# Performance work log

Hardware: AMD Instinct MI355X
Metric: run time of the kernel (lower is better)

Reference implementation:

```python
import jax, jax.numpy as jnp
import numpy as np

WS = 2   # window_size
NH = 8   # num_heads


def window_attn(x, Wqkv, bqkv, scale, ws=WS, nh=NH):
    # x: (B, H, W, C) -> tiny ws*ws-token windowed MHA, faithful to torch reshape order
    B, H, W, C = x.shape
    hg, wg = H // ws, W // ws
    hd = C // nh
    xw = x.reshape(B, hg, ws, wg, ws, C).transpose(0, 1, 3, 2, 4, 5)  # (B,hg,wg,ws,ws,C)
    qkv = (xw @ Wqkv + bqkv).reshape(B, hg * wg, ws * ws, 3, nh, hd)
    q, k, v = jnp.transpose(qkv, (3, 0, 1, 4, 2, 5))  # each (B,G,nh,n,hd), n=ws*ws
    attn = jax.nn.softmax(jnp.einsum('bgnqd,bgnkd->bgnqk', q, k) * scale, axis=-1)
    o = jnp.einsum('bgnqk,bgnkd->bgnqd', attn, v)
    o = o.transpose(0, 1, 3, 2, 4).reshape(B, hg, wg, ws, ws, C)
    return o.transpose(0, 1, 3, 2, 4, 5).reshape(B, H, W, C)


def reference(x, Wqkv, bqkv, Wproj, bproj):
    B, C, H, W = x.shape
    scale = (C // NH) ** (-0.5)
    xr = x.reshape(B, H, W, C)  # raw reshape (NOT a transpose) -- faithful to source

    # --- Global path ---
    g = window_attn(xr, Wqkv, bqkv, scale) @ Wproj + bproj

    # --- Local path ---
    l = xr.reshape(B, C, H, W)                         # raw reshape, as in source
    l = l.reshape(B, C, H // 2, 2, W // 2, 2).mean(axis=(3, 5))  # AvgPool2d(2)
    h, w = H // 2, W // 2
    l = l.reshape(B, h, w, C)                          # raw reshape, as in source
    l = window_attn(l, Wqkv, bqkv, scale)
    l = l.reshape(B, C, h, w)                          # raw reshape, as in source
    # attn_x: reflect-pad top by 1, AvgPool2d((2,1), stride=1)
    px = jnp.pad(l, ((0, 0), (0, 0), (1, 0), (0, 0)), mode='reflect')
    lx = 0.5 * (px[:, :, :-1, :] + px[:, :, 1:, :])
    # attn_y: reflect-pad right by 1, AvgPool2d((1,2), stride=1)
    py = jnp.pad(l, ((0, 0), (0, 0), (0, 0), (0, 1)), mode='reflect')
    ly = 0.5 * (py[..., :-1] + py[..., 1:])
    # bilinear upsample x2, align_corners=False (half-pixel, matches jax.image.resize)
    l = jax.image.resize(lx + ly, (B, C, H, W), method='bilinear')
    l = l.reshape(B, H, W, C)                          # raw reshape, as in source

    return (g + l).transpose(0, 3, 1, 2)  # (B, C, H, W)


def setup_inputs() -> dict:
    key = jax.random.key(0)
    k1, k2, k3, k4, k5 = jax.random.split(key, 5)
    B, C, H, W = 4, 512, 128, 128
    x = jax.random.normal(k1, (B, C, H, W), dtype=jnp.float32)
    Wqkv = jax.random.normal(k2, (C, 3 * C), dtype=jnp.float32) * 0.02
    bqkv = jax.random.normal(k3, (3 * C,), dtype=jnp.float32) * 0.02
    Wproj = jax.random.normal(k4, (C, C), dtype=jnp.float32) * 0.02
    bproj = jax.random.normal(k5, (C,), dtype=jnp.float32) * 0.02
    return {'x': x, 'Wqkv': Wqkv, 'bqkv': bqkv, 'Wproj': Wproj, 'bproj': bproj}
```

## Files before the change

kernel.cpp:

```cpp
#include <hip/hip_runtime.h>

typedef float f32x4 __attribute__((ext_vector_type(4)));
typedef float f32x2 __attribute__((ext_vector_type(2)));
typedef __bf16 bf16x8 __attribute__((ext_vector_type(8)));
typedef __bf16 bf16x4 __attribute__((ext_vector_type(4)));

__device__ __forceinline__ void gll16(const void* g, void* l) {
  __builtin_amdgcn_global_load_lds(
      (const __attribute__((address_space(1))) uint32_t*)g,
      (__attribute__((address_space(3))) uint32_t*)l, 16, 0, 0);
}

__global__ __launch_bounds__(256) void gemm_bf16_k512(
    const __bf16* __restrict__ A, const __bf16* __restrict__ BT,
    const float* __restrict__ bias, __bf16* __restrict__ C, int N, int gx)
{
  __shared__ __bf16 sh[16384];
  __bf16* As = sh;
  __bf16* Bs = sh + 8192;
  const int tid = threadIdx.x;
  const int wave = tid >> 6, lane = tid & 63;
  const int wr = (wave >> 1) * 64, wc = (wave & 1) * 64;
  const int l15 = lane & 15, l4 = lane >> 4;

  int lin = blockIdx.x;
  int olin = (lin & 7) * ((int)gridDim.x >> 3) + (lin >> 3);
  int bn = olin % gx, bm = olin / gx;
  const long arow0 = (long)bm * 128;
  const long brow0 = (long)bn * 128;

  const int srow = wave * 8 + (lane >> 3);
  const int scp8 = (lane & 7) * 8;

  f32x4 acc[4][4] = {};

  for (int kt = 0; kt < 512; kt += 64) {
    #pragma unroll
    for (int i = 0; i < 4; i++) {
      int row = srow + i * 32;
      int gc = scp8 ^ ((row & 7) * 8);
      gll16(A  + (arow0 + row) * 512 + kt + gc, (char*)As + i * 4096 + wave * 1024);
      gll16(BT + (brow0 + row) * 512 + kt + gc, (char*)Bs + i * 4096 + wave * 1024);
    }
    __syncthreads();
    #pragma unroll
    for (int kk = 0; kk < 2; kk++) {
      bf16x8 af[4], bfr[4];
      #pragma unroll
      for (int m = 0; m < 4; m++) {
        int row = wr + m * 16 + l15;
        int cp8 = ((kk * 4 + l4) * 8) ^ ((row & 7) * 8);
        af[m] = *(const bf16x8*)&As[row * 64 + cp8];
      }
      #pragma unroll
      for (int n = 0; n < 4; n++) {
        int row = wc + n * 16 + l15;
        int cp8 = ((kk * 4 + l4) * 8) ^ ((row & 7) * 8);
        bfr[n] = *(const bf16x8*)&Bs[row * 64 + cp8];
      }
      #pragma unroll
      for (int m = 0; m < 4; m++)
        #pragma unroll
        for (int n = 0; n < 4; n++)
          acc[m][n] = __builtin_amdgcn_mfma_f32_16x16x32_bf16(bfr[n], af[m], acc[m][n], 0, 0, 0);
    }
    __syncthreads();
  }

  #pragma unroll
  for (int n = 0; n < 4; n++) {
    f32x4 bv = *(const f32x4*)(bias + brow0 + wc + n * 16 + l4 * 4);
    #pragma unroll
    for (int m = 0; m < 4; m++) {
      int row = wr + m * 16 + l15;
      int colb = (wc + n * 16 + l4 * 4) * 2;
      int byte = row * 256 + (colb ^ ((row & 7) << 4));
      bf16x4 o;
      #pragma unroll
      for (int k = 0; k < 4; k++) o[k] = (__bf16)(acc[m][n][k] + bv[k]);
      *(bf16x4*)((char*)sh + byte) = o;
    }
  }
  __syncthreads();
  {
    int row = tid >> 1;
    int halfs = (tid & 1) * 8;
    __bf16* gdst = C + (arow0 + row) * (long)N + brow0 + halfs * 8;
    #pragma unroll
    for (int k = 0; k < 8; k++) {
      int s = halfs + k;
      int slot = (s & 8) | ((s ^ row) & 7);
      bf16x8 v = *(const bf16x8*)((const char*)sh + row * 256 + slot * 16);
      *(bf16x8*)(gdst + k * 8) = v;
    }
  }
}

__global__ __launch_bounds__(256) void attn4(
    const __bf16* __restrict__ qkv, __bf16* __restrict__ o,
    int nwin, int wg, int Wimg, int wpb, int bst)
{
  int tid = blockIdx.x * 256 + threadIdx.x;
  int m = tid & 3;
  int head = (tid >> 2) & 7;
  int win = tid >> 5;
  if (win >= nwin) return;
  int b = win / wpb, wrm = win % wpb;
  int i = wrm / wg, j = wrm % wg;
  int t0 = b * bst + 2 * i * Wimg + 2 * j;
  int tn[4] = { t0, t0 + 1, t0 + Wimg, t0 + Wimg + 1 };
  int trow = tn[m];
  const int co = head * 64;

  float qf[64];
  #pragma unroll
  for (int c = 0; c < 8; c++) {
    bf16x8 v = *(const bf16x8*)(qkv + (long)trow * 1536 + co + c * 8);
    #pragma unroll
    for (int e = 0; e < 8; e++) qf[c * 8 + e] = (float)v[e];
  }

  float s[4];
  #pragma unroll
  for (int n = 0; n < 4; n++) {
    float acc = 0.f;
    #pragma unroll
    for (int c = 0; c < 8; c++) {
      bf16x8 kv = *(const bf16x8*)(qkv + (long)tn[n] * 1536 + 512 + co + c * 8);
      #pragma unroll
      for (int e = 0; e < 8; e++) acc += qf[c * 8 + e] * (float)kv[e];
    }
    s[n] = acc * 0.125f;
  }

  float mx = fmaxf(fmaxf(s[0], s[1]), fmaxf(s[2], s[3]));
  float e0 = __expf(s[0] - mx), e1 = __expf(s[1] - mx),
        e2 = __expf(s[2] - mx), e3 = __expf(s[3] - mx);
  float inv = 1.f / (e0 + e1 + e2 + e3);
  float w4[4] = { e0 * inv, e1 * inv, e2 * inv, e3 * inv };

  float of[64] = {};
  #pragma unroll
  for (int n = 0; n < 4; n++) {
    float wn = w4[n];
    #pragma unroll
    for (int c = 0; c < 8; c++) {
      bf16x8 vv = *(const bf16x8*)(qkv + (long)tn[n] * 1536 + 1024 + co + c * 8);
      #pragma unroll
      for (int e = 0; e < 8; e++) of[c * 8 + e] += wn * (float)vv[e];
    }
  }

  #pragma unroll
  for (int c = 0; c < 8; c++) {
    bf16x8 ov;
    #pragma unroll
    for (int e = 0; e < 8; e++) ov[e] = (__bf16)of[c * 8 + e];
    *(bf16x8*)(o + (long)trow * 512 + co + c * 8) = ov;
  }
}

__global__ __launch_bounds__(256) void transpose_f32_bf16(
    const float* __restrict__ in, __bf16* __restrict__ out, int K, int N)
{
  __shared__ float t[64][65];
  int n0 = blockIdx.x * 64, k0 = blockIdx.y * 64;
  int tid = threadIdx.x;
  int nl4 = (tid & 15) * 4, kl = tid >> 4;
  #pragma unroll
  for (int p = 0; p < 4; p++) {
    int kk = kl + p * 16;
    f32x4 v = *(const f32x4*)(in + (long)(k0 + kk) * N + n0 + nl4);
    t[kk][nl4 + 0] = v.x; t[kk][nl4 + 1] = v.y; t[kk][nl4 + 2] = v.z; t[kk][nl4 + 3] = v.w;
  }
  __syncthreads();
  int ks = tid & 63, wv = tid >> 6;
  #pragma unroll
  for (int p = 0; p < 16; p++) {
    int nn = wv * 16 + p;
    out[(long)(n0 + nn) * K + k0 + ks] = (__bf16)t[ks][nn];
  }
}

__global__ __launch_bounds__(256) void convpool(const float* __restrict__ x,
    __bf16* __restrict__ Xbf, __bf16* __restrict__ P)
{
  int t = blockIdx.x * 256 + threadIdx.x;
  int j8 = (t & 15) * 8;
  int i2 = (t >> 4) & 63;
  long bc = t >> 10;
  const float* r0 = x + bc * 16384 + (2 * i2) * 128 + j8;
  f32x4 a0 = *(const f32x4*)r0,         a1 = *(const f32x4*)(r0 + 4);
  f32x4 b0 = *(const f32x4*)(r0 + 128), b1 = *(const f32x4*)(r0 + 132);
  bf16x8 xa, xb;
  xa[0] = (__bf16)a0.x; xa[1] = (__bf16)a0.y; xa[2] = (__bf16)a0.z; xa[3] = (__bf16)a0.w;
  xa[4] = (__bf16)a1.x; xa[5] = (__bf16)a1.y; xa[6] = (__bf16)a1.z; xa[7] = (__bf16)a1.w;
  xb[0] = (__bf16)b0.x; xb[1] = (__bf16)b0.y; xb[2] = (__bf16)b0.z; xb[3] = (__bf16)b0.w;
  xb[4] = (__bf16)b1.x; xb[5] = (__bf16)b1.y; xb[6] = (__bf16)b1.z; xb[7] = (__bf16)b1.w;
  *(bf16x8*)(Xbf + bc * 16384 + (2 * i2) * 128 + j8) = xa;
  *(bf16x8*)(Xbf + bc * 16384 + (2 * i2) * 128 + 128 + j8) = xb;
  bf16x4 p;
  p[0] = (__bf16)((a0.x + a0.y + b0.x + b0.y) * 0.25f);
  p[1] = (__bf16)((a0.z + a0.w + b0.z + b0.w) * 0.25f);
  p[2] = (__bf16)((a1.x + a1.y + b1.x + b1.y) * 0.25f);
  p[3] = (__bf16)((a1.z + a1.w + b1.z + b1.w) * 0.25f);
  *(bf16x4*)(P + bc * 4096 + i2 * 64 + (t & 15) * 4) = p;
}

__global__ void skern(const __bf16* __restrict__ l, float* __restrict__ s)
{
  int tid = blockIdx.x * 256 + threadIdx.x;
  int j = tid & 63, i = (tid >> 6) & 63;
  long bc = tid >> 12;
  const __bf16* base = l + bc * 4096;
  int im1 = (i == 0) ? 1 : i - 1;
  int jp1 = (j == 63) ? 62 : j + 1;
  float v = 0.5f * (float)base[im1 * 64 + j] + (float)base[i * 64 + j]
          + 0.5f * (float)base[i * 64 + jp1];
  s[tid] = v;
}

__global__ __launch_bounds__(256) void final_v2(
    const __bf16* __restrict__ G, const float* __restrict__ S, float* __restrict__ out)
{
  __shared__ float Sl[8192];
  __shared__ float t[64][65];
  int b = blockIdx.z;
  int p0 = blockIdx.y * 64, c0 = blockIdx.x * 64;
  int tid = threadIdx.x;

  int k2 = blockIdx.y;
  const float* Sb = S + (long)b * 2097152 + (long)k2 * 8192;
  #pragma unroll
  for (int i = 0; i < 8; i++)
    *(f32x4*)&Sl[i * 1024 + tid * 4] = *(const f32x4*)(Sb + i * 1024 + tid * 4);
  __syncthreads();

  int cl4 = (tid & 15) * 4, pl = tid >> 4;
  const __bf16* Gb = G + ((long)b * 16384 + p0) * 512 + c0;
  #pragma unroll
  for (int q2 = 0; q2 < 4; q2++) {
    int pp = pl + q2 * 16;
    bf16x4 g = *(const bf16x4*)(Gb + (long)pp * 512 + cl4);
    int qbase = (p0 + pp) * 512 + c0 + cl4;
    #pragma unroll
    for (int e = 0; e < 4; e++) {
      int q = qbase + e;
      int lc = (q >> 14) & 1;
      int r = q & 16383, hh = r >> 7, ww = r & 127;
      const float* sb = Sl + lc * 4096;
      int i0, i1, j0, j1; float wi0, wi1, wj0, wj1;
      if (hh & 1) { i0 = hh >> 1; i1 = (i0 < 63) ? i0 + 1 : 63; wi0 = 0.75f; wi1 = 0.25f; }
      else        { i1 = hh >> 1; i0 = (i1 > 0) ? i1 - 1 : 0;   wi0 = 0.25f; wi1 = 0.75f; }
      if (ww & 1) { j0 = ww >> 1; j1 = (j0 < 63) ? j0 + 1 : 63; wj0 = 0.75f; wj1 = 0.25f; }
      else        { j1 = ww >> 1; j0 = (j1 > 0) ? j1 - 1 : 0;   wj0 = 0.25f; wj1 = 0.75f; }
      float up = wi0 * (wj0 * sb[i0 * 64 + j0] + wj1 * sb[i0 * 64 + j1])
               + wi1 * (wj0 * sb[i1 * 64 + j0] + wj1 * sb[i1 * 64 + j1]);
      t[pp][cl4 + e] = (float)g[e] + up;
    }
  }
  __syncthreads();
  int l15b = tid & 15, hi = (tid >> 4) & 3, wv = tid >> 6;
  float* ob = out + (long)b * 8388608 + (long)c0 * 16384 + p0;
  #pragma unroll
  for (int it = 0; it < 4; it++) {
    int cc = wv * 16 + it * 4 + hi;
    f32x4 v;
    v.x = t[l15b * 4 + 0][cc]; v.y = t[l15b * 4 + 1][cc];
    v.z = t[l15b * 4 + 2][cc]; v.w = t[l15b * 4 + 3][cc];
    *(f32x4*)(ob + (long)cc * 16384 + l15b * 4) = v;
  }
}

extern "C" void kernel_launch(void* const* d_in, const int* in_sizes, int n_in,
                              void* d_out, int out_size, void* d_ws, size_t ws_size,
                              hipStream_t stream)
{
  const float* x     = (const float*)d_in[0];
  const float* Wqkv  = (const float*)d_in[1];
  const float* bqkv  = (const float*)d_in[2];
  const float* Wproj = (const float*)d_in[3];
  const float* bproj = (const float*)d_in[4];
  float* out = (float*)d_out;

  char* w = (char*)d_ws;
  __bf16* WqkvT  = (__bf16*)w;  w += (size_t)1536 * 512 * 2;
  __bf16* WprojT = (__bf16*)w;  w += (size_t)512 * 512 * 2;
  __bf16* Xbf    = (__bf16*)w;  w += (size_t)65536 * 512 * 2;
  __bf16* G      = Xbf;
  __bf16* P      = (__bf16*)w;  w += (size_t)2048 * 4096 * 2;

  bool batched = ws_size >= ((size_t)356 << 20);
  size_t mchunk = batched ? 65536 : 16384;
  __bf16* QKVbuf = (__bf16*)w;  w += mchunk * 1536 * 2;
  __bf16* Obuf   = (__bf16*)w;
  float*  S      = (float*)QKVbuf;

  transpose_f32_bf16<<<dim3(24, 8), 256, 0, stream>>>(Wqkv, WqkvT, 512, 1536);
  transpose_f32_bf16<<<dim3(8, 8), 256, 0, stream>>>(Wproj, WprojT, 512, 512);
  convpool<<<8192, 256, 0, stream>>>(x, Xbf, P);

  int nch = batched ? 1 : 4;
  int mrows = (int)mchunk;
  for (int c = 0; c < nch; c++) {
    const __bf16* Ac = Xbf + (size_t)c * 16384 * 512;
    gemm_bf16_k512<<<12 * (mrows / 128), 256, 0, stream>>>(Ac, WqkvT, bqkv, QKVbuf, 1536, 12);
    attn4<<<(mrows / 4) * 32 / 256, 256, 0, stream>>>(
        QKVbuf, Obuf, mrows / 4, 64, 128, 4096, 16384);
    gemm_bf16_k512<<<4 * (mrows / 128), 256, 0, stream>>>(
        Obuf, WprojT, bproj, G + (size_t)c * 16384 * 512, 512, 4);
  }

  gemm_bf16_k512<<<12 * 128, 256, 0, stream>>>(P, WqkvT, bqkv, QKVbuf, 1536, 12);
  attn4<<<512, 256, 0, stream>>>(QKVbuf, Obuf, 4096, 32, 64, 1024, 4096);
  skern<<<8388608 / 256, 256, 0, stream>>>(Obuf, S);

  final_v2<<<dim3(8, 256, 4), 256, 0, stream>>>(G, S, out);
}
```

Measured before the change: 528.5 us.

## Double-buffer GEMM LDS tiles and store epilogue directly to global

The bf16 K=512 GEMM now keeps two LDS buffers for the A and B tiles. It issues the global-to-LDS loads for the next k-tile before computing the current one, and needs one barrier per iteration instead of two. The epilogue no longer stages the output through LDS with a swizzle. Each lane adds the bias and writes its 4-element bf16 fragments straight to global memory. LDS use doubles to 64 KB per block, which may lower occupancy, and the direct 8-byte stores are less coalesced than the old 16-byte row stores.

Result: faster. 493.1 us (-6.7%).

```diff
diff --git a/kernel.cpp b/kernel.cpp
--- a/kernel.cpp
+++ b/kernel.cpp
@@ -15,9 +15,8 @@
     const __bf16* __restrict__ A, const __bf16* __restrict__ BT,
     const float* __restrict__ bias, __bf16* __restrict__ C, int N, int gx)
 {
-  __shared__ __bf16 sh[16384];
-  __bf16* As = sh;
-  __bf16* Bs = sh + 8192;
+  __shared__ __bf16 As[2][8192];
+  __shared__ __bf16 Bs[2][8192];
   const int tid = threadIdx.x;
   const int wave = tid >> 6, lane = tid & 63;
   const int wr = (wave >> 1) * 64, wc = (wave & 1) * 64;
@@ -34,15 +33,22 @@
 
   f32x4 acc[4][4] = {};
 
-  for (int kt = 0; kt < 512; kt += 64) {
+  auto stage = [&](int p, int kt) {
     #pragma unroll
     for (int i = 0; i < 4; i++) {
       int row = srow + i * 32;
       int gc = scp8 ^ ((row & 7) * 8);
-      gll16(A  + (arow0 + row) * 512 + kt + gc, (char*)As + i * 4096 + wave * 1024);
-      gll16(BT + (brow0 + row) * 512 + kt + gc, (char*)Bs + i * 4096 + wave * 1024);
-    }
-    __syncthreads();
+      gll16(A  + (arow0 + row) * 512 + kt + gc, (char*)As[p] + i * 4096 + wave * 1024);
+      gll16(BT + (brow0 + row) * 512 + kt + gc, (char*)Bs[p] + i * 4096 + wave * 1024);
+    }
+  };
+
+  stage(0, 0);
+  __syncthreads();
+
+  for (int t = 0; t < 8; t++) {
+    int cur = t & 1;
+    if (t < 7) stage(cur ^ 1, (t + 1) * 64);
     #pragma unroll
     for (int kk = 0; kk < 2; kk++) {
       bf16x8 af[4], bfr[4];
@@ -50,13 +56,13 @@
       for (int m = 0; m < 4; m++) {
         int row = wr + m * 16 + l15;
         int cp8 = ((kk * 4 + l4) * 8) ^ ((row & 7) * 8);
-        af[m] = *(const bf16x8*)&As[row * 64 + cp8];
+        af[m] = *(const bf16x8*)&As[cur][row * 64 + cp8];
       }
       #pragma unroll
       for (int n = 0; n < 4; n++) {
         int row = wc + n * 16 + l15;
         int cp8 = ((kk * 4 + l4) * 8) ^ ((row & 7) * 8);
-        bfr[n] = *(const bf16x8*)&Bs[row * 64 + cp8];
+        bfr[n] = *(const bf16x8*)&Bs[cur][row * 64 + cp8];
       }
       #pragma unroll
       for (int m = 0; m < 4; m++)
@@ -64,34 +70,20 @@
         for (int n = 0; n < 4; n++)
           acc[m][n] = __builtin_amdgcn_mfma_f32_16x16x32_bf16(bfr[n], af[m], acc[m][n], 0, 0, 0);
     }
-    __syncthreads();
-  }
-
-  #pragma unroll
-  for (int n = 0; n < 4; n++) {
-    f32x4 bv = *(const f32x4*)(bias + brow0 + wc + n * 16 + l4 * 4);
-    #pragma unroll
-    for (int m = 0; m < 4; m++) {
-      int row = wr + m * 16 + l15;
-      int colb = (wc + n * 16 + l4 * 4) * 2;
-      int byte = row * 256 + (colb ^ ((row & 7) << 4));
+    if (t < 7) __syncthreads();
+  }
+
+  #pragma unroll
+  for (int m = 0; m < 4; m++) {
+    long row = arow0 + wr + m * 16 + l15;
+    __bf16* crow = C + row * (long)N + brow0;
+    #pragma unroll
+    for (int n = 0; n < 4; n++) {
+      f32x4 bv = *(const f32x4*)(bias + brow0 + wc + n * 16 + l4 * 4);
       bf16x4 o;
       #pragma unroll
       for (int k = 0; k < 4; k++) o[k] = (__bf16)(acc[m][n][k] + bv[k]);
-      *(bf16x4*)((char*)sh + byte) = o;
-    }
-  }
-  __syncthreads();
-  {
-    int row = tid >> 1;
-    int halfs = (tid & 1) * 8;
-    __bf16* gdst = C + (arow0 + row) * (long)N + brow0 + halfs * 8;
-    #pragma unroll
-    for (int k = 0; k < 8; k++) {
-      int s = halfs + k;
-      int slot = (s & 8) | ((s ^ row) & 7);
-      bf16x8 v = *(const bf16x8*)((const char*)sh + row * 256 + slot * 16);
-      *(bf16x8*)(gdst + k * 8) = v;
+      *(bf16x4*)(crow + wc + n * 16 + l4 * 4) = o;
     }
   }
 }
```
